# Kernel optimization log

Measured on AMD Instinct MI355X. Metric: run time of the kernel, lower is better.

Reference implementation:

```python
import jax, jax.numpy as jnp
import numpy as np

N = 500_000      # nodes per snapshot (production scale)
E = 2_000_000    # edges (unused in math: ChebConv K=1)
F_IN = 165       # elliptic tx features
HID = 32
NUM_CLASSES = 2


def setup_inputs() -> dict:
    key = jax.random.key(0)
    ks = jax.random.split(key, 24)
    s = 0.05
    d = {
        "x": jax.random.normal(ks[0], (N, F_IN), jnp.float32),
        "edge_index": jax.random.randint(ks[1], (2, E), 0, N, dtype=jnp.int64),
        "edge_weight": jnp.ones((E,), jnp.float32),
        "h": 0.1 * jax.random.normal(ks[2], (N, HID), jnp.float32),
        "c": 0.1 * jax.random.normal(ks[3], (N, HID), jnp.float32),
    }
    # GCLSTM parameters: input projections W_* [F_IN,HID], biases b_* [1,HID],
    # per-gate ChebConv(K=1) == Linear(HID,HID): Wc_* [HID,HID], bc_* [HID]
    names_W = ["W_i", "W_f", "W_c", "W_o"]
    names_b = ["b_i", "b_f", "b_c", "b_o"]
    names_Wc = ["Wc_i", "Wc_f", "Wc_c", "Wc_o"]
    names_bc = ["bc_i", "bc_f", "bc_c", "bc_o"]
    k = 4
    for n in names_W:
        d[n] = s * jax.random.normal(ks[k], (F_IN, HID), jnp.float32); k += 1
    for n in names_b:
        d[n] = jnp.zeros((1, HID), jnp.float32)
    for n in names_Wc:
        d[n] = s * jax.random.normal(ks[k], (HID, HID), jnp.float32); k += 1
    for n in names_bc:
        d[n] = jnp.zeros((HID,), jnp.float32)
    d["W_lin"] = s * jax.random.normal(ks[k], (HID, NUM_CLASSES), jnp.float32)
    d["b_lin"] = jnp.zeros((NUM_CLASSES,), jnp.float32)
    return d


def reference(x, edge_index, edge_weight, h, c,
              W_i, W_f, W_c, W_o, b_i, b_f, b_c, b_o,
              Wc_i, Wc_f, Wc_c, Wc_o, bc_i, bc_f, bc_c, bc_o,
              W_lin, b_lin):
    # GCLSTM cell with K=1 ChebConv per gate (ChebConv(K=1) == Linear, edges unused).
    i = jax.nn.sigmoid(x @ W_i + h @ Wc_i + bc_i + b_i)   # input gate   [N,HID]
    f = jax.nn.sigmoid(x @ W_f + h @ Wc_f + bc_f + b_f)   # forget gate
    g = jnp.tanh(x @ W_c + h @ Wc_c + bc_c + b_c)         # cell candidate
    c_0 = f * c + i * g                                   # new cell state
    o = jax.nn.sigmoid(x @ W_o + h @ Wc_o + bc_o + b_o)   # output gate
    h_0 = o * jnp.tanh(c_0)                               # new hidden state
    y = jax.nn.relu(h_0) @ W_lin + b_lin                  # classifier [N,2]
    return (y, h_0, c_0)
```

## Files before the change

kernel.cpp:

```cpp
#include <hip/hip_runtime.h>

#define F_IN 165
#define HID  32
#define TROWS 32
#define XBYTES (TROWS * F_IN * 4)
#define XUNITS 21
#define HCBYTES (TROWS * HID * 4)
#define HCUNITS 4
#define HOFF   (XUNITS * 1024)
#define COFF   (HOFF + HCBYTES)
#define BUFSZ  (COFF + HCBYTES)
#define PYOFF  (2 * BUFSZ)

typedef __attribute__((ext_vector_type(8))) __bf16 bf16x8;
typedef __attribute__((ext_vector_type(4))) float  f32x4;

typedef __attribute__((address_space(1))) void as1_void;
typedef __attribute__((address_space(3))) void as3_void;

__device__ __forceinline__ void gload_lds16(const void* g, void* l) {
    __builtin_amdgcn_global_load_lds(
        reinterpret_cast<as1_void*>(reinterpret_cast<uintptr_t>(g)),
        reinterpret_cast<as3_void*>((uint32_t)reinterpret_cast<uintptr_t>(l)),
        16, 0, 0);
}

__device__ __forceinline__ float fast_sigmoid(float x) {
    return __builtin_amdgcn_rcpf(1.f + __builtin_amdgcn_exp2f(-1.4426950408889634f * x));
}
__device__ __forceinline__ float fast_tanh(float x) {
    return 1.f - 2.f * __builtin_amdgcn_rcpf(1.f + __builtin_amdgcn_exp2f(2.8853900817779268f * x));
}

#define FRAG_BYTES 57344

struct PrepParams {
    const float *W0, *W1, *W2, *W3;
    const float *Wc0, *Wc1, *Wc2, *Wc3;
    const float *b0, *b1, *b2, *b3;
    const float *bc0, *bc1, *bc2, *bc3;
    char* ws;
};

__global__ void gclstm_prep(PrepParams pp) {
    int t = blockIdx.x * 256 + threadIdx.x;
    if (t < 56 * 64) {
        int slot = t >> 6, l = t & 63;
        int ks = slot >> 3, g = (slot >> 1) & 3, hf = slot & 1;
        int cl = l & 15, q = l >> 4;
        const float* W = (ks < 6)
            ? (g==0 ? pp.W0  : g==1 ? pp.W1  : g==2 ? pp.W2  : pp.W3)
            : (g==0 ? pp.Wc0 : g==1 ? pp.Wc1 : g==2 ? pp.Wc2 : pp.Wc3);
        bf16x8 v;
#pragma unroll
        for (int j = 0; j < 8; ++j) {
            float f = 0.f;
            if (ks < 6) {
                int k = ks * 32 + q * 8 + j;
                if (k < F_IN) f = W[k * HID + hf * 16 + cl];
            } else {
                int k = q * 8 + j;
                f = W[k * HID + hf * 16 + cl];
            }
            v[j] = (__bf16)f;
        }
        *(bf16x8*)(pp.ws + slot * 1024 + l * 16) = v;
    } else if (t < 56 * 64 + 128) {
        int i = t - 56 * 64;
        int g = i >> 5, col = i & 31;
        const float* B  = g==0 ? pp.b0  : g==1 ? pp.b1  : g==2 ? pp.b2  : pp.b3;
        const float* Bc = g==0 ? pp.bc0 : g==1 ? pp.bc1 : g==2 ? pp.bc2 : pp.bc3;
        ((float*)(pp.ws + FRAG_BYTES))[i] = B[col] + Bc[col];
    }
}

struct Params {
    const float *x, *h, *c, *Wl, *bl;
    const char* ws;
    float *y, *h0o, *c0o;
    int n, nt;
};

__device__ __forceinline__ void stage_tile(const Params& p, char* smem, int bb,
                                           int tt, int w, int l, bool last) {
    char* buf = smem + bb * BUFSZ;
    if (w < 3) {
        const char* xc = (const char*)p.x + (size_t)tt * XBYTES + (size_t)l * 16;
#pragma unroll
        for (int i = 0; i < 7; ++i) {
            int u = w * 7 + i;
            if (u != 20 || !last || l < 40)
                gload_lds16(xc + u * 1024, buf + u * 1024);
        }
    } else {
        const char* hc = (const char*)p.h + (size_t)tt * HCBYTES + (size_t)l * 16;
        const char* cc = (const char*)p.c + (size_t)tt * HCBYTES + (size_t)l * 16;
#pragma unroll
        for (int i = 0; i < HCUNITS; ++i) {
            gload_lds16(hc + i * 1024, buf + HOFF + i * 1024);
            gload_lds16(cc + i * 1024, buf + COFF + i * 1024);
        }
    }
}

__global__ __launch_bounds__(256, 2) void gclstm_main(Params p) {
    __shared__ char smem[PYOFF + 512];
    float* py = (float*)(smem + PYOFF);

    const int tid = threadIdx.x;
    const int w   = tid >> 6;
    const int sub = w >> 1, hf = w & 1;
    const int l   = tid & 63;
    const int cl  = l & 15, q = l >> 4;
    const int col = hf * 16 + cl;

    bf16x8 bw[4][7];
#pragma unroll
    for (int ks = 0; ks < 7; ++ks)
#pragma unroll
        for (int g = 0; g < 4; ++g)
            bw[g][ks] = *(const bf16x8*)(p.ws + (ks * 8 + g * 2 + hf) * 1024 + l * 16);

    const float* biasT = (const float*)(p.ws + FRAG_BYTES);
    float bias[4];
#pragma unroll
    for (int g = 0; g < 4; ++g) bias[g] = biasT[g * 32 + col];
    const float wl0 = p.Wl[col * 2 + 0];
    const float wl1 = p.Wl[col * 2 + 1];
    const float bl0 = p.bl[0], bl1 = p.bl[1];

    const int nt = p.nt, stride = gridDim.x;
    int t = blockIdx.x;
    if (t >= nt) return;

    stage_tile(p, smem, 0, t, w, l, t == nt - 1);
    asm volatile("s_waitcnt vmcnt(0)" ::: "memory");
    __builtin_amdgcn_s_barrier();
    asm volatile("" ::: "memory");

    int cur = 0;
    while (true) {
        const int tn = t + stride;
        const bool more = (tn < nt);
        if (more) stage_tile(p, smem, cur ^ 1, tn, w, l, tn == nt - 1);

        const char*  buf = smem + cur * BUFSZ;
        const float* xb  = (const float*)buf;
        const float* hb  = (const float*)(buf + HOFF);
        const float* cb  = (const float*)(buf + COFF);
        const int lrow = sub * 16 + cl;
        const int rb   = lrow * F_IN;

        bf16x8 af[7];
#pragma unroll
        for (int ks = 0; ks < 5; ++ks) {
            float v[8];
#pragma unroll
            for (int j = 0; j < 8; ++j) v[j] = xb[rb + ks * 32 + q * 8 + j];
#pragma unroll
            for (int j = 0; j < 8; ++j) af[ks][j] = (__bf16)v[j];
        }
        {
            bool qz = (q == 0);
            float t0 = xb[rb + 160], t1 = xb[rb + 161], t2 = xb[rb + 162];
            float t3 = xb[rb + 163], t4 = xb[rb + 164];
            af[5][0] = (__bf16)(qz ? t0 : 0.f);
            af[5][1] = (__bf16)(qz ? t1 : 0.f);
            af[5][2] = (__bf16)(qz ? t2 : 0.f);
            af[5][3] = (__bf16)(qz ? t3 : 0.f);
            af[5][4] = (__bf16)(qz ? t4 : 0.f);
            af[5][5] = (__bf16)0.f; af[5][6] = (__bf16)0.f; af[5][7] = (__bf16)0.f;
        }
        {
            const float* hr = hb + lrow * HID + q * 8;
            float4 hA = *(const float4*)hr;
            float4 hB = *(const float4*)(hr + 4);
            af[6][0]=(__bf16)hA.x; af[6][1]=(__bf16)hA.y; af[6][2]=(__bf16)hA.z; af[6][3]=(__bf16)hA.w;
            af[6][4]=(__bf16)hB.x; af[6][5]=(__bf16)hB.y; af[6][6]=(__bf16)hB.z; af[6][7]=(__bf16)hB.w;
        }

        f32x4 acc[4];
#pragma unroll
        for (int g = 0; g < 4; ++g) acc[g] = (f32x4){0.f, 0.f, 0.f, 0.f};
#pragma unroll
        for (int ks = 0; ks < 7; ++ks)
#pragma unroll
            for (int g = 0; g < 4; ++g)
                acc[g] = __builtin_amdgcn_mfma_f32_16x16x32_bf16(af[ks], bw[g][ks], acc[g], 0, 0, 0);

        const int  drow  = sub * 16 + 4 * q;
        const long gbase = (long)t * TROWS;
#pragma unroll
        for (int jj = 0; jj < 4; ++jj) {
            float iv = fast_sigmoid(acc[0][jj] + bias[0]);
            float fv = fast_sigmoid(acc[1][jj] + bias[1]);
            float gv = fast_tanh   (acc[2][jj] + bias[2]);
            float ov = fast_sigmoid(acc[3][jj] + bias[3]);
            float cvv = cb[(drow + jj) * HID + col];
            float c0 = fv * cvv + iv * gv;
            float h0 = ov * fast_tanh(c0);
            long grow = gbase + drow + jj;
            p.c0o[grow * HID + col] = c0;
            p.h0o[grow * HID + col] = h0;
            float rl = fmaxf(h0, 0.f);
            float r0 = rl * wl0, r1 = rl * wl1;
            r0 += __shfl_xor(r0, 1); r0 += __shfl_xor(r0, 2);
            r0 += __shfl_xor(r0, 4); r0 += __shfl_xor(r0, 8);
            r1 += __shfl_xor(r1, 1); r1 += __shfl_xor(r1, 2);
            r1 += __shfl_xor(r1, 4); r1 += __shfl_xor(r1, 8);
            if (cl == 0) {
                py[((sub * 2 + hf) * 16 + 4 * q + jj) * 2 + 0] = r0;
                py[((sub * 2 + hf) * 16 + 4 * q + jj) * 2 + 1] = r1;
            }
        }
        asm volatile("s_waitcnt lgkmcnt(0)" ::: "memory");
        __builtin_amdgcn_s_barrier();
        asm volatile("" ::: "memory");
        if (l < 16) {
            int v = w * 16 + l;
            int r = v >> 1, k = v & 1;
            int s2 = r >> 4, r16 = r & 15;
            float yv = py[((s2 * 2 + 0) * 16 + r16) * 2 + k]
                     + py[((s2 * 2 + 1) * 16 + r16) * 2 + k]
                     + (k ? bl1 : bl0);
            p.y[gbase * 2 + v] = yv;
        }

        if (!more) break;
        asm volatile("s_waitcnt vmcnt(9)" ::: "memory");
        __builtin_amdgcn_s_barrier();
        asm volatile("" ::: "memory");
        cur ^= 1; t = tn;
    }
}

extern "C" void kernel_launch(void* const* d_in, const int* in_sizes, int n_in,
                              void* d_out, int out_size, void* d_ws, size_t ws_size,
                              hipStream_t stream) {
    PrepParams pp;
    pp.W0  = (const float*)d_in[5];
    pp.W1  = (const float*)d_in[6];
    pp.W2  = (const float*)d_in[7];
    pp.W3  = (const float*)d_in[8];
    pp.b0  = (const float*)d_in[9];
    pp.b1  = (const float*)d_in[10];
    pp.b2  = (const float*)d_in[11];
    pp.b3  = (const float*)d_in[12];
    pp.Wc0 = (const float*)d_in[13];
    pp.Wc1 = (const float*)d_in[14];
    pp.Wc2 = (const float*)d_in[15];
    pp.Wc3 = (const float*)d_in[16];
    pp.bc0 = (const float*)d_in[17];
    pp.bc1 = (const float*)d_in[18];
    pp.bc2 = (const float*)d_in[19];
    pp.bc3 = (const float*)d_in[20];
    pp.ws  = (char*)d_ws;
    hipLaunchKernelGGL(gclstm_prep, dim3(15), dim3(256), 0, stream, pp);

    Params p;
    p.x  = (const float*)d_in[0];
    p.h  = (const float*)d_in[3];
    p.c  = (const float*)d_in[4];
    p.Wl = (const float*)d_in[21];
    p.bl = (const float*)d_in[22];
    p.ws = (const char*)d_ws;

    const int n = in_sizes[0] / F_IN;
    p.n  = n;
    p.nt = n / TROWS;

    float* out = (float*)d_out;
    p.y   = out;
    p.h0o = out + (long)n * 2;
    p.c0o = out + (long)n * 2 + (long)n * HID;

    hipLaunchKernelGGL(gclstm_main, dim3(1024), dim3(256), 0, stream, p);
}
```

Measured before the change: 129.6 us.

## Switch to triple-buffered LDS ring with one block per CU

```diff
diff --git a/kernel.cpp b/kernel.cpp
--- a/kernel.cpp
+++ b/kernel.cpp
@@ -6,11 +6,11 @@
 #define XBYTES (TROWS * F_IN * 4)
 #define XUNITS 21
 #define HCBYTES (TROWS * HID * 4)
-#define HCUNITS 4
 #define HOFF   (XUNITS * 1024)
 #define COFF   (HOFF + HCBYTES)
 #define BUFSZ  (COFF + HCBYTES)
-#define PYOFF  (2 * BUFSZ)
+#define RING   3
+#define PYOFF  (RING * BUFSZ)
 
 typedef __attribute__((ext_vector_type(8))) __bf16 bf16x8;
 typedef __attribute__((ext_vector_type(4))) float  f32x4;
@@ -81,9 +81,9 @@
     int n, nt;
 };
 
-__device__ __forceinline__ void stage_tile(const Params& p, char* smem, int bb,
+__device__ __forceinline__ void stage_tile(const Params& p, char* smem, int slot,
                                            int tt, int w, int l, bool last) {
-    char* buf = smem + bb * BUFSZ;
+    char* buf = smem + slot * BUFSZ;
     if (w < 3) {
         const char* xc = (const char*)p.x + (size_t)tt * XBYTES + (size_t)l * 16;
 #pragma unroll
@@ -96,14 +96,14 @@
         const char* hc = (const char*)p.h + (size_t)tt * HCBYTES + (size_t)l * 16;
         const char* cc = (const char*)p.c + (size_t)tt * HCBYTES + (size_t)l * 16;
 #pragma unroll
-        for (int i = 0; i < HCUNITS; ++i) {
+        for (int i = 0; i < 4; ++i) {
             gload_lds16(hc + i * 1024, buf + HOFF + i * 1024);
             gload_lds16(cc + i * 1024, buf + COFF + i * 1024);
         }
     }
 }
 
-__global__ __launch_bounds__(256, 2) void gclstm_main(Params p) {
+__global__ __launch_bounds__(256, 1) void gclstm_main(Params p) {
     __shared__ char smem[PYOFF + 512];
     float* py = (float*)(smem + PYOFF);
 
@@ -134,15 +134,22 @@
     if (t >= nt) return;
 
     stage_tile(p, smem, 0, t, w, l, t == nt - 1);
+    {
+        int t1 = t + stride;
+        stage_tile(p, smem, 1, t1 < nt ? t1 : 0, w, l, t1 == nt - 1);
+    }
     asm volatile("s_waitcnt vmcnt(0)" ::: "memory");
-    __builtin_amdgcn_s_barrier();
-    asm volatile("" ::: "memory");
 
     int cur = 0;
     while (true) {
-        const int tn = t + stride;
-        const bool more = (tn < nt);
-        if (more) stage_tile(p, smem, cur ^ 1, tn, w, l, tn == nt - 1);
+        {
+            int t2 = t + 2 * stride;
+            stage_tile(p, smem, (cur + 2) % RING, t2 < nt ? t2 : 0, w, l, t2 == nt - 1);
+        }
+        if (w == 3) asm volatile("s_waitcnt vmcnt(34)" ::: "memory");
+        else        asm volatile("s_waitcnt vmcnt(32)" ::: "memory");
+        __builtin_amdgcn_s_barrier();
+        asm volatile("" ::: "memory");
 
         const char*  buf = smem + cur * BUFSZ;
         const float* xb  = (const float*)buf;
@@ -216,6 +223,7 @@
         asm volatile("s_waitcnt lgkmcnt(0)" ::: "memory");
         __builtin_amdgcn_s_barrier();
         asm volatile("" ::: "memory");
+
         if (l < 16) {
             int v = w * 16 + l;
             int r = v >> 1, k = v & 1;
@@ -226,11 +234,9 @@
             p.y[gbase * 2 + v] = yv;
         }
 
-        if (!more) break;
-        asm volatile("s_waitcnt vmcnt(9)" ::: "memory");
-        __builtin_amdgcn_s_barrier();
-        asm volatile("" ::: "memory");
-        cur ^= 1; t = tn;
+        t += stride;
+        if (t >= nt) break;
+        cur = (cur + 1) % RING;
     }
 }
 
@@ -274,5 +280,5 @@
     p.h0o = out + (long)n * 2;
     p.c0o = out + (long)n * 2 + (long)n * HID;
 
-    hipLaunchKernelGGL(gclstm_main, dim3(1024), dim3(256), 0, stream, p);
-}
+    hipLaunchKernelGGL(gclstm_main, dim3(256), dim3(256), 0, stream, p);
+}
```

Result: slower. 168.4 us (+29.9%).

## Halve tile rows to 16, use 128-thread blocks, and XOR-swizzle h/c LDS staging

Applied to the files above, without the earlier changes.

```diff
diff --git a/kernel.cpp b/kernel.cpp
--- a/kernel.cpp
+++ b/kernel.cpp
@@ -2,11 +2,10 @@
 
 #define F_IN 165
 #define HID  32
-#define TROWS 32
+#define TROWS 16
 #define XBYTES (TROWS * F_IN * 4)
-#define XUNITS 21
+#define XUNITS 11
 #define HCBYTES (TROWS * HID * 4)
-#define HCUNITS 4
 #define HOFF   (XUNITS * 1024)
 #define COFF   (HOFF + HCBYTES)
 #define BUFSZ  (COFF + HCBYTES)
@@ -81,45 +80,50 @@
     int n, nt;
 };
 
-__device__ __forceinline__ void stage_tile(const Params& p, char* smem, int bb,
+__device__ __forceinline__ void stage_tile(const Params& p, char* smem, int slot,
                                            int tt, int w, int l, bool last) {
-    char* buf = smem + bb * BUFSZ;
-    if (w < 3) {
-        const char* xc = (const char*)p.x + (size_t)tt * XBYTES + (size_t)l * 16;
-#pragma unroll
-        for (int i = 0; i < 7; ++i) {
-            int u = w * 7 + i;
-            if (u != 20 || !last || l < 40)
-                gload_lds16(xc + u * 1024, buf + u * 1024);
-        }
+    char* buf = smem + slot * BUFSZ;
+    const char* xc = (const char*)p.x + (size_t)tt * XBYTES + (size_t)l * 16;
+    if (w == 0) {
+#pragma unroll
+        for (int i = 0; i < 7; ++i)
+            gload_lds16(xc + i * 1024, buf + i * 1024);
     } else {
-        const char* hc = (const char*)p.h + (size_t)tt * HCBYTES + (size_t)l * 16;
-        const char* cc = (const char*)p.c + (size_t)tt * HCBYTES + (size_t)l * 16;
-#pragma unroll
-        for (int i = 0; i < HCUNITS; ++i) {
-            gload_lds16(hc + i * 1024, buf + HOFF + i * 1024);
-            gload_lds16(cc + i * 1024, buf + COFF + i * 1024);
+#pragma unroll
+        for (int i = 7; i < 11; ++i) {
+            if (i != 10 || !last || l < 20)
+                gload_lds16(xc + i * 1024, buf + i * 1024);
+        }
+        const int r = l >> 3;
+        const int o = (l & 7) * 16;
+        const int osw = o ^ (r << 4);
+        const char* hb = (const char*)p.h + (size_t)tt * HCBYTES;
+        const char* cc = (const char*)p.c + (size_t)tt * HCBYTES;
+#pragma unroll
+        for (int i = 0; i < 2; ++i) {
+            int srcoff = (i * 8 + r) * 128 + osw;
+            gload_lds16(hb + srcoff, buf + HOFF + i * 1024 + l * 16);
+            gload_lds16(cc + srcoff, buf + COFF + i * 1024 + l * 16);
         }
     }
 }
 
-__global__ __launch_bounds__(256, 2) void gclstm_main(Params p) {
-    __shared__ char smem[PYOFF + 512];
+__global__ __launch_bounds__(128, 2) void gclstm_main(Params p) {
+    __shared__ char smem[PYOFF + 256];
     float* py = (float*)(smem + PYOFF);
 
     const int tid = threadIdx.x;
     const int w   = tid >> 6;
-    const int sub = w >> 1, hf = w & 1;
     const int l   = tid & 63;
     const int cl  = l & 15, q = l >> 4;
-    const int col = hf * 16 + cl;
+    const int col = w * 16 + cl;
 
     bf16x8 bw[4][7];
 #pragma unroll
     for (int ks = 0; ks < 7; ++ks)
 #pragma unroll
         for (int g = 0; g < 4; ++g)
-            bw[g][ks] = *(const bf16x8*)(p.ws + (ks * 8 + g * 2 + hf) * 1024 + l * 16);
+            bw[g][ks] = *(const bf16x8*)(p.ws + (ks * 8 + g * 2 + w) * 1024 + l * 16);
 
     const float* biasT = (const float*)(p.ws + FRAG_BYTES);
     float bias[4];
@@ -146,10 +150,7 @@
 
         const char*  buf = smem + cur * BUFSZ;
         const float* xb  = (const float*)buf;
-        const float* hb  = (const float*)(buf + HOFF);
-        const float* cb  = (const float*)(buf + COFF);
-        const int lrow = sub * 16 + cl;
-        const int rb   = lrow * F_IN;
+        const int rb = cl * F_IN;
 
         bf16x8 af[7];
 #pragma unroll
@@ -172,9 +173,10 @@
             af[5][5] = (__bf16)0.f; af[5][6] = (__bf16)0.f; af[5][7] = (__bf16)0.f;
         }
         {
-            const float* hr = hb + lrow * HID + q * 8;
-            float4 hA = *(const float4*)hr;
-            float4 hB = *(const float4*)(hr + 4);
+            const int s  = (cl & 7) << 4;
+            const char* hrow = buf + HOFF + cl * 128;
+            float4 hA = *(const float4*)(hrow + ((q * 32)      ^ s));
+            float4 hB = *(const float4*)(hrow + ((q * 32 + 16) ^ s));
             af[6][0]=(__bf16)hA.x; af[6][1]=(__bf16)hA.y; af[6][2]=(__bf16)hA.z; af[6][3]=(__bf16)hA.w;
             af[6][4]=(__bf16)hB.x; af[6][5]=(__bf16)hB.y; af[6][6]=(__bf16)hB.z; af[6][7]=(__bf16)hB.w;
         }
@@ -188,18 +190,18 @@
             for (int g = 0; g < 4; ++g)
                 acc[g] = __builtin_amdgcn_mfma_f32_16x16x32_bf16(af[ks], bw[g][ks], acc[g], 0, 0, 0);
 
-        const int  drow  = sub * 16 + 4 * q;
         const long gbase = (long)t * TROWS;
 #pragma unroll
         for (int jj = 0; jj < 4; ++jj) {
+            const int r = 4 * q + jj;
             float iv = fast_sigmoid(acc[0][jj] + bias[0]);
             float fv = fast_sigmoid(acc[1][jj] + bias[1]);
             float gv = fast_tanh   (acc[2][jj] + bias[2]);
             float ov = fast_sigmoid(acc[3][jj] + bias[3]);
-            float cvv = cb[(drow + jj) * HID + col];
+            float cvv = *(const float*)(buf + COFF + r * 128 + ((col * 4) ^ ((r & 7) << 4)));
             float c0 = fv * cvv + iv * gv;
             float h0 = ov * fast_tanh(c0);
-            long grow = gbase + drow + jj;
+            long grow = gbase + r;
             p.c0o[grow * HID + col] = c0;
             p.h0o[grow * HID + col] = h0;
             float rl = fmaxf(h0, 0.f);
@@ -209,19 +211,18 @@
             r1 += __shfl_xor(r1, 1); r1 += __shfl_xor(r1, 2);
             r1 += __shfl_xor(r1, 4); r1 += __shfl_xor(r1, 8);
             if (cl == 0) {
-                py[((sub * 2 + hf) * 16 + 4 * q + jj) * 2 + 0] = r0;
-                py[((sub * 2 + hf) * 16 + 4 * q + jj) * 2 + 1] = r1;
+                py[(w * 16 + r) * 2 + 0] = r0;
+                py[(w * 16 + r) * 2 + 1] = r1;
             }
         }
         asm volatile("s_waitcnt lgkmcnt(0)" ::: "memory");
         __builtin_amdgcn_s_barrier();
         asm volatile("" ::: "memory");
+
         if (l < 16) {
             int v = w * 16 + l;
             int r = v >> 1, k = v & 1;
-            int s2 = r >> 4, r16 = r & 15;
-            float yv = py[((s2 * 2 + 0) * 16 + r16) * 2 + k]
-                     + py[((s2 * 2 + 1) * 16 + r16) * 2 + k]
+            float yv = py[(0 * 16 + r) * 2 + k] + py[(1 * 16 + r) * 2 + k]
                      + (k ? bl1 : bl0);
             p.y[gbase * 2 + v] = yv;
         }
@@ -274,5 +275,5 @@
     p.h0o = out + (long)n * 2;
     p.c0o = out + (long)n * 2 + (long)n * HID;
 
-    hipLaunchKernelGGL(gclstm_main, dim3(1024), dim3(256), 0, stream, p);
-}
+    hipLaunchKernelGGL(gclstm_main, dim3(1280), dim3(128), 0, stream, p);
+}
```

Measured after the change: 157.2 us. +21.3%, slower.

## Load h and c directly to registers, shrink LDS to fit three blocks per CU

Applied to the files above, without the earlier changes.

```diff
diff --git a/kernel.cpp b/kernel.cpp
--- a/kernel.cpp
+++ b/kernel.cpp
@@ -5,11 +5,7 @@
 #define TROWS 32
 #define XBYTES (TROWS * F_IN * 4)
 #define XUNITS 21
-#define HCBYTES (TROWS * HID * 4)
-#define HCUNITS 4
-#define HOFF   (XUNITS * 1024)
-#define COFF   (HOFF + HCBYTES)
-#define BUFSZ  (COFF + HCBYTES)
+#define BUFSZ  (XUNITS * 1024)
 #define PYOFF  (2 * BUFSZ)
 
 typedef __attribute__((ext_vector_type(8))) __bf16 bf16x8;
@@ -81,29 +77,25 @@
     int n, nt;
 };
 
-__device__ __forceinline__ void stage_tile(const Params& p, char* smem, int bb,
-                                           int tt, int w, int l, bool last) {
+__device__ __forceinline__ void stage_x(const Params& p, char* smem, int bb,
+                                        int tt, int w, int l, bool last) {
     char* buf = smem + bb * BUFSZ;
-    if (w < 3) {
-        const char* xc = (const char*)p.x + (size_t)tt * XBYTES + (size_t)l * 16;
-#pragma unroll
-        for (int i = 0; i < 7; ++i) {
-            int u = w * 7 + i;
+    const char* xc = (const char*)p.x + (size_t)tt * XBYTES + (size_t)l * 16;
+    if (w == 0) {
+#pragma unroll
+        for (int i = 0; i < 6; ++i)
+            gload_lds16(xc + i * 1024, buf + i * 1024);
+    } else {
+#pragma unroll
+        for (int i = 0; i < 5; ++i) {
+            int u = 1 + w * 5 + i;
             if (u != 20 || !last || l < 40)
                 gload_lds16(xc + u * 1024, buf + u * 1024);
         }
-    } else {
-        const char* hc = (const char*)p.h + (size_t)tt * HCBYTES + (size_t)l * 16;
-        const char* cc = (const char*)p.c + (size_t)tt * HCBYTES + (size_t)l * 16;
-#pragma unroll
-        for (int i = 0; i < HCUNITS; ++i) {
-            gload_lds16(hc + i * 1024, buf + HOFF + i * 1024);
-            gload_lds16(cc + i * 1024, buf + COFF + i * 1024);
-        }
     }
 }
 
-__global__ __launch_bounds__(256, 2) void gclstm_main(Params p) {
+__global__ __launch_bounds__(256, 3) void gclstm_main(Params p) {
     __shared__ char smem[PYOFF + 512];
     float* py = (float*)(smem + PYOFF);
 
@@ -133,7 +125,10 @@
     int t = blockIdx.x;
     if (t >= nt) return;
 
-    stage_tile(p, smem, 0, t, w, l, t == nt - 1);
+    const int lrow = sub * 16 + cl;
+    const int drow = sub * 16 + 4 * q;
+
+    stage_x(p, smem, 0, t, w, l, t == nt - 1);
     asm volatile("s_waitcnt vmcnt(0)" ::: "memory");
     __builtin_amdgcn_s_barrier();
     asm volatile("" ::: "memory");
@@ -142,14 +137,24 @@
     while (true) {
         const int tn = t + stride;
         const bool more = (tn < nt);
-        if (more) stage_tile(p, smem, cur ^ 1, tn, w, l, tn == nt - 1);
-
-        const char*  buf = smem + cur * BUFSZ;
-        const float* xb  = (const float*)buf;
-        const float* hb  = (const float*)(buf + HOFF);
-        const float* cb  = (const float*)(buf + COFF);
-        const int lrow = sub * 16 + cl;
-        const int rb   = lrow * F_IN;
+        const long gbase = (long)t * TROWS;
+
+        float4 hA, hB;
+        float cv[4];
+        {
+            const float* hr = p.h + (gbase + lrow) * HID + q * 8;
+            hA = *(const float4*)hr;
+            hB = *(const float4*)(hr + 4);
+#pragma unroll
+            for (int jj = 0; jj < 4; ++jj)
+                cv[jj] = p.c[(gbase + drow + jj) * HID + col];
+        }
+        __builtin_amdgcn_sched_barrier(0);
+        if (more) stage_x(p, smem, cur ^ 1, tn, w, l, tn == nt - 1);
+        __builtin_amdgcn_sched_barrier(0);
+
+        const float* xb = (const float*)(smem + cur * BUFSZ);
+        const int rb = lrow * F_IN;
 
         bf16x8 af[7];
 #pragma unroll
@@ -172,9 +177,6 @@
             af[5][5] = (__bf16)0.f; af[5][6] = (__bf16)0.f; af[5][7] = (__bf16)0.f;
         }
         {
-            const float* hr = hb + lrow * HID + q * 8;
-            float4 hA = *(const float4*)hr;
-            float4 hB = *(const float4*)(hr + 4);
             af[6][0]=(__bf16)hA.x; af[6][1]=(__bf16)hA.y; af[6][2]=(__bf16)hA.z; af[6][3]=(__bf16)hA.w;
             af[6][4]=(__bf16)hB.x; af[6][5]=(__bf16)hB.y; af[6][6]=(__bf16)hB.z; af[6][7]=(__bf16)hB.w;
         }
@@ -188,16 +190,13 @@
             for (int g = 0; g < 4; ++g)
                 acc[g] = __builtin_amdgcn_mfma_f32_16x16x32_bf16(af[ks], bw[g][ks], acc[g], 0, 0, 0);
 
-        const int  drow  = sub * 16 + 4 * q;
-        const long gbase = (long)t * TROWS;
 #pragma unroll
         for (int jj = 0; jj < 4; ++jj) {
             float iv = fast_sigmoid(acc[0][jj] + bias[0]);
             float fv = fast_sigmoid(acc[1][jj] + bias[1]);
             float gv = fast_tanh   (acc[2][jj] + bias[2]);
             float ov = fast_sigmoid(acc[3][jj] + bias[3]);
-            float cvv = cb[(drow + jj) * HID + col];
-            float c0 = fv * cvv + iv * gv;
+            float c0 = fv * cv[jj] + iv * gv;
             float h0 = ov * fast_tanh(c0);
             long grow = gbase + drow + jj;
             p.c0o[grow * HID + col] = c0;
@@ -216,6 +215,7 @@
         asm volatile("s_waitcnt lgkmcnt(0)" ::: "memory");
         __builtin_amdgcn_s_barrier();
         asm volatile("" ::: "memory");
+
         if (l < 16) {
             int v = w * 16 + l;
             int r = v >> 1, k = v & 1;
@@ -274,5 +274,5 @@
     p.h0o = out + (long)n * 2;
     p.c0o = out + (long)n * 2 + (long)n * HID;
 
-    hipLaunchKernelGGL(gclstm_main, dim3(1024), dim3(256), 0, stream, p);
-}
+    hipLaunchKernelGGL(gclstm_main, dim3(768), dim3(256), 0, stream, p);
+}
```

New measurement: 201.9 us. 1.56x slower.
